# Kernel tuning notes

Measured on AMD Instinct MI355X. Metric: run time of the kernel, lower is better.

Reference implementation:

```python
import jax, jax.numpy as jnp
import numpy as np

K = 5       # kernel_size
UP = 2      # up_factor
EPS = 1e-5  # BatchNorm eps (eval mode)


def _conv(x, w, pad, dil=1):
    return jax.lax.conv_general_dilated(
        x, w, (1, 1), [(pad, pad), (pad, pad)], rhs_dilation=(dil, dil),
        dimension_numbers=('NCHW', 'OIHW', 'NCHW'))


def _bn(x, g, b, m, v):
    inv = g / jnp.sqrt(v + EPS)
    return x * inv[:, None, None] + (b - m * inv)[:, None, None]


def _bilinear(x, oh, ow):
    # torch F.interpolate(mode='bilinear', align_corners=False)
    N, C, H, W = x.shape
    def coords(out_s, in_s):
        s = in_s / out_s
        src = (jnp.arange(out_s, dtype=jnp.float32) + 0.5) * s - 0.5
        src = jnp.clip(src, 0.0, in_s - 1)
        i0 = jnp.floor(src).astype(jnp.int32)
        i1 = jnp.minimum(i0 + 1, in_s - 1)
        return i0, i1, src - i0
    y0, y1, wy = coords(oh, H)
    x0, x1, wx = coords(ow, W)
    g = lambda yi, xi: x[:, :, yi][:, :, :, xi]  # (N,C,oh,ow)
    top = g(y0, x0) * (1 - wx) + g(y0, x1) * wx
    bot = g(y1, x0) * (1 - wx) + g(y1, x1) * wx
    return top * (1 - wy)[:, None] + bot * wy[:, None]


def _unfold(x):
    # F.unfold(k=5, pad=2) reshaped to (N, C, K*K, H, W); channel-major (c, kh, kw)
    p = K // 2
    N, C, H, W = x.shape
    xp = jnp.pad(x, ((0, 0), (0, 0), (p, p), (p, p)))
    patches = [xp[:, :, i:i + H, j:j + W] for i in range(K) for j in range(K)]
    return jnp.stack(patches, axis=2)


def setup_inputs() -> dict:
    key = jax.random.key(0)
    ks = jax.random.split(key, 8)
    N, C, H, W = 2, 256, 48, 48
    Cc = C // 4
    Cout = 256
    d = {}
    d['x'] = jax.random.normal(ks[0], (N, C, H, W), dtype=jnp.float32)
    d['compress_w'] = jax.random.normal(ks[1], (Cc, C, 1, 1), dtype=jnp.float32) * 0.05
    d['g1'] = jnp.ones((Cc,), jnp.float32)
    d['b1'] = jnp.zeros((Cc,), jnp.float32)
    d['m1'] = jax.random.normal(ks[2], (Cc,), dtype=jnp.float32) * 0.1
    d['v1'] = jax.random.uniform(ks[3], (Cc,), minval=0.5, maxval=1.5, dtype=jnp.float32)
    d['ke1_w'] = jax.random.normal(ks[4], (Cc, Cc, 3, 3), dtype=jnp.float32) * 0.05
    d['gk'] = jnp.ones((Cc,), jnp.float32)
    d['bk'] = jnp.zeros((Cc,), jnp.float32)
    d['mk'] = jax.random.normal(ks[5], (Cc,), dtype=jnp.float32) * 0.1
    d['vk'] = jax.random.uniform(ks[6], (Cc,), minval=0.5, maxval=1.5, dtype=jnp.float32)
    d['ke2_w'] = jax.random.normal(ks[7], (UP * UP * K * K, Cc, 3, 3), dtype=jnp.float32) * 0.05
    d['proj_w'] = jax.random.normal(jax.random.fold_in(key, 10), (Cout, C, 1, 1), dtype=jnp.float32) * 0.05
    d['g2'] = jnp.ones((Cout,), jnp.float32)
    d['b2'] = jnp.zeros((Cout,), jnp.float32)
    d['m2'] = jax.random.normal(jax.random.fold_in(key, 11), (Cout,), dtype=jnp.float32) * 0.1
    d['v2'] = jax.random.uniform(jax.random.fold_in(key, 12), (Cout,), minval=0.5, maxval=1.5, dtype=jnp.float32)
    return d


def reference(x, compress_w, g1, b1, m1, v1, ke1_w, gk, bk, mk, vk, ke2_w,
              proj_w, g2, b2, m2, v2):
    N, C, H, W = x.shape
    oh, ow = H * UP, W * UP
    # kernel prediction branch
    comp = jax.nn.relu(_bn(_conv(x, compress_w, 0), g1, b1, m1, v1))
    k1 = jax.nn.relu(_bn(_conv(comp, ke1_w, 2, dil=2), gk, bk, mk, vk))
    kernel = _conv(k1, ke2_w, 1)                               # (N, UP^2*K^2, H, W)
    kernel = jax.nn.softmax(kernel.reshape(N, UP * UP, K * K, H, W), axis=2)
    # content reassembly
    x_up = jnp.repeat(jnp.repeat(x, UP, axis=2), UP, axis=3)
    x_unf = _unfold(x_up)                                      # (N, C, K^2, oh, ow)
    k_up = _bilinear(kernel.reshape(N, UP * UP * K * K, H, W), oh, ow)
    k_up = k_up.reshape(N, UP * UP, K * K, oh, ow)
    out = jnp.einsum('nckhw,nukhw->nuchw', x_unf, k_up)        # (N, UP^2, C, oh, ow)
    # view (N, UP^2*C, oh, ow) then pixel_shuffle(UP)
    out = out.reshape(N, UP * UP * C, oh, ow)
    out = out.reshape(N, C, UP, UP, oh, ow)
    out = out.transpose(0, 1, 4, 2, 5, 3).reshape(N, C, oh * UP, ow * UP)
    out = jax.nn.relu(_bn(_conv(out, proj_w, 0), g2, b2, m2, v2))
    return out
```

## Files before the change

### kernel.cpp

```cpp
#include <hip/hip_runtime.h>

#define EPSB 1e-5f

typedef __attribute__((ext_vector_type(8))) short bf16x8;
typedef __attribute__((ext_vector_type(4))) float f32x4;

__device__ __forceinline__ unsigned short f2b(float f) {
  union { float f; unsigned u; } cv; cv.f = f;
  unsigned r = cv.u + 0x7FFFu + ((cv.u >> 16) & 1u);
  return (unsigned short)(r >> 16);
}

__global__ __launch_bounds__(256) void k_head(
    const float* __restrict__ x, const float* __restrict__ cw,
    const float* __restrict__ g1, const float* __restrict__ b1,
    const float* __restrict__ m1, const float* __restrict__ v1,
    const float* __restrict__ k1w, const float* __restrict__ k2w,
    const float* __restrict__ pw,
    unsigned short* __restrict__ comp_t, unsigned short* __restrict__ pwb,
    unsigned short* __restrict__ wt1, unsigned short* __restrict__ wt2) {
  int bid = blockIdx.x, t = threadIdx.x;
  if (bid < 288) {
    __shared__ unsigned short wl[16640];
    for (int f = t; f < 16384; f += 256) {
      int co = f >> 8, ci = f & 255;
      wl[ci * 65 + co] = f2b(cw[f]);
    }
    __syncthreads();
    int idx = bid * 256 + t;
    int co2 = (idx & 31) * 2;
    int pg = idx >> 5;
    int n = pg / 1152;
    int pix0 = (pg % 1152) * 2;
    const float* xp = x + (size_t)n * 256 * 2304 + pix0;
    float a00 = 0.f, a01 = 0.f, a10 = 0.f, a11 = 0.f;
    for (int ci = 0; ci < 256; ++ci) {
      float2 xv = *(const float2*)(xp + (size_t)ci * 2304);
      unsigned pr = *(const unsigned*)&wl[ci * 65 + co2];
      union { unsigned u; float f; } wa, wb;
      wa.u = pr << 16; wb.u = pr & 0xffff0000u;
      a00 = fmaf(xv.x, wa.f, a00); a01 = fmaf(xv.y, wa.f, a01);
      a10 = fmaf(xv.x, wb.f, a10); a11 = fmaf(xv.y, wb.f, a11);
    }
    float iv0 = g1[co2] / sqrtf(v1[co2] + EPSB);
    float iv1 = g1[co2 + 1] / sqrtf(v1[co2 + 1] + EPSB);
    float c0b = b1[co2] - m1[co2] * iv0;
    float c1b = b1[co2 + 1] - m1[co2 + 1] * iv1;
    float o00 = fmaxf(fmaf(a00, iv0, c0b), 0.f), o01 = fmaxf(fmaf(a01, iv0, c0b), 0.f);
    float o10 = fmaxf(fmaf(a10, iv1, c1b), 0.f), o11 = fmaxf(fmaf(a11, iv1, c1b), 0.f);
    int r = pix0 / 48, c = pix0 % 48;
    unsigned short* ob = comp_t + ((size_t)n * 2704 + (r + 2) * 52 + (c + 2)) * 64 + co2;
    *(unsigned*)&ob[0]  = (unsigned)f2b(o00) | ((unsigned)f2b(o10) << 16);
    *(unsigned*)&ob[64] = (unsigned)f2b(o01) | ((unsigned)f2b(o11) << 16);
  } else if (bid < 388) {
    int i = (bid - 288) * 256 + t;
    int n = i / 12800, r = i % 12800;
    int bp = r >> 5, c32 = r & 31;
    int rr, cc;
    if (bp < 104) { rr = bp / 52; cc = bp % 52; }
    else if (bp >= 296) { rr = 50 + (bp - 296) / 52; cc = (bp - 296) % 52; }
    else { int q = bp - 104; rr = 2 + (q >> 2); int c4 = q & 3; cc = (c4 < 2) ? c4 : c4 + 48; }
    ((unsigned*)comp_t)[((size_t)n * 2704 + rr * 52 + cc) * 32 + c32] = 0u;
  } else {
    int i2 = (bid - 388) * 256 + t;
    if (i2 < 65536) {
      pwb[i2] = f2b(pw[i2]);
    } else if (i2 < 102400) {
      int a = i2 - 65536;
      int co = a / 576, k = a % 576, tap = k >> 6, ci = k & 63;
      wt1[a] = f2b(k1w[co * 576 + ci * 9 + tap]);
    } else {
      int c2 = i2 - 102400;
      int co = c2 / 576, k = c2 % 576, tap = k >> 6, ci = k & 63;
      wt2[c2] = (co < 100) ? f2b(k2w[co * 576 + ci * 9 + tap]) : (unsigned short)0;
    }
  }
}

__global__ __launch_bounds__(128) void k_ke1(
    const unsigned short* __restrict__ comp_t, const unsigned short* __restrict__ wt1,
    const float* __restrict__ gk, const float* __restrict__ bk,
    const float* __restrict__ mk, const float* __restrict__ vk,
    unsigned short* __restrict__ k1_t) {
  int bid = blockIdx.x, t = threadIdx.x;
  if (bid >= 192) {
    int j = (bid - 192) * 128 + t;
    int n = j / 6272, r = j % 6272;
    int bp = r >> 5, c32 = r & 31;
    int rr, cc;
    if (bp < 50) { rr = 0; cc = bp; }
    else if (bp >= 146) { rr = 49; cc = bp - 146; }
    else { int q = bp - 50; rr = 1 + (q >> 1); cc = (q & 1) * 49; }
    ((unsigned*)k1_t)[((size_t)n * 2500 + rr * 50 + cc) * 32 + c32] = 0u;
    return;
  }
  __shared__ unsigned short sA[16640];
  int n = bid / 96, rem = bid % 96;
  int y = rem >> 1, coh = rem & 1;
  const unsigned short* src = comp_t + ((size_t)n * 52 + y) * 52 * 64;
  for (int f = t; f < 2080; f += 128) {
    int g = f >> 3, ci0 = (f & 7) * 8;
    int cc = g % 52, rr = g / 52;
    bf16x8 vv = *(const bf16x8*)&src[(rr * 52 + cc) * 64 + ci0];
    int ba = (((rr * 52 + cc) * 64 + ci0) * 2) ^ ((cc & 7) << 4);
    *(bf16x8*)((char*)sA + ba) = vv;
  }
  __syncthreads();
  int wid = t >> 6, l = t & 63, l15 = l & 15, lg = l >> 4;
  f32x4 acc[3];
  acc[0] = acc[1] = acc[2] = (f32x4){0.f, 0.f, 0.f, 0.f};
  const unsigned short* arow = wt1 + (size_t)(coh * 32 + wid * 16 + l15) * 576;
#pragma unroll
  for (int kbi = 0; kbi < 18; ++kbi) {
    int tap = kbi >> 1;
    int ky = tap / 3, kx = tap % 3;
    int ci0 = (kbi & 1) * 32 + lg * 8;
    bf16x8 afr = *(const bf16x8*)&arow[kbi * 32 + lg * 8];
#pragma unroll
    for (int nt = 0; nt < 3; ++nt) {
      int col = nt * 16 + l15 + 2 * kx;
      int ba = (((2 * ky * 52 + col) * 64 + ci0) * 2) ^ ((col & 7) << 4);
      bf16x8 bfr = *(const bf16x8*)((char*)sA + ba);
      acc[nt] = __builtin_amdgcn_mfma_f32_16x16x32_bf16(afr, bfr, acc[nt], 0, 0, 0);
    }
  }
  unsigned short* dst = k1_t + ((size_t)n * 50 + (y + 1)) * 50 * 64;
  int co0 = coh * 32 + wid * 16 + lg * 4;
  float s0 = gk[co0] / sqrtf(vk[co0] + EPSB);
  float s1 = gk[co0 + 1] / sqrtf(vk[co0 + 1] + EPSB);
  float s2 = gk[co0 + 2] / sqrtf(vk[co0 + 2] + EPSB);
  float s3 = gk[co0 + 3] / sqrtf(vk[co0 + 3] + EPSB);
  float d0 = bk[co0] - mk[co0] * s0;
  float d1 = bk[co0 + 1] - mk[co0 + 1] * s1;
  float d2 = bk[co0 + 2] - mk[co0 + 2] * s2;
  float d3 = bk[co0 + 3] - mk[co0 + 3] * s3;
#pragma unroll
  for (int nt = 0; nt < 3; ++nt) {
    int px = nt * 16 + l15;
    ushort4 pk;
    pk.x = f2b(fmaxf(fmaf(acc[nt][0], s0, d0), 0.f));
    pk.y = f2b(fmaxf(fmaf(acc[nt][1], s1, d1), 0.f));
    pk.z = f2b(fmaxf(fmaf(acc[nt][2], s2, d2), 0.f));
    pk.w = f2b(fmaxf(fmaf(acc[nt][3], s3, d3), 0.f));
    *(ushort4*)&dst[(px + 1) * 64 + co0] = pk;
  }
}

__global__ __launch_bounds__(128) void k_ke2(
    const unsigned short* __restrict__ k1_t, const unsigned short* __restrict__ wt2,
    float* __restrict__ kern_t) {
  __shared__ unsigned short sA[9600];
  int bid = blockIdx.x, t = threadIdx.x;
  int n = bid / 96, rem = bid % 96;
  int y = rem >> 1, coh = rem & 1;
  const unsigned short* src = k1_t + ((size_t)n * 50 + y) * 50 * 64;
  for (int f = t; f < 1200; f += 128) {
    int g = f >> 3, ci0 = (f & 7) * 8;
    int cc = g % 50, rr = g / 50;
    bf16x8 vv = *(const bf16x8*)&src[(rr * 50 + cc) * 64 + ci0];
    int ba = (((rr * 50 + cc) * 64 + ci0) * 2) ^ ((cc & 7) << 4);
    *(bf16x8*)((char*)sA + ba) = vv;
  }
  __syncthreads();
  int wid = t >> 6, l = t & 63, l15 = l & 15, lg = l >> 4;
  f32x4 acc[2][3];
#pragma unroll
  for (int mi = 0; mi < 2; ++mi)
#pragma unroll
    for (int nt = 0; nt < 3; ++nt) acc[mi][nt] = (f32x4){0.f, 0.f, 0.f, 0.f};
#pragma unroll
  for (int kbi = 0; kbi < 18; ++kbi) {
    int tap = kbi >> 1;
    int ky = tap / 3, kx = tap % 3;
    int ci0 = (kbi & 1) * 32 + lg * 8;
    bf16x8 afr[2];
#pragma unroll
    for (int mi = 0; mi < 2; ++mi)
      afr[mi] = *(const bf16x8*)&wt2[(size_t)(coh * 64 + (wid * 2 + mi) * 16 + l15) * 576 + kbi * 32 + lg * 8];
#pragma unroll
    for (int nt = 0; nt < 3; ++nt) {
      int col = nt * 16 + l15 + kx;
      int ba = (((ky * 50 + col) * 64 + ci0) * 2) ^ ((col & 7) << 4);
      bf16x8 bfr = *(const bf16x8*)((char*)sA + ba);
      acc[0][nt] = __builtin_amdgcn_mfma_f32_16x16x32_bf16(afr[0], bfr, acc[0][nt], 0, 0, 0);
      acc[1][nt] = __builtin_amdgcn_mfma_f32_16x16x32_bf16(afr[1], bfr, acc[1][nt], 0, 0, 0);
    }
  }
#pragma unroll
  for (int mi = 0; mi < 2; ++mi) {
    int co0 = coh * 64 + (wid * 2 + mi) * 16 + lg * 4;
    if (co0 < 112) {
#pragma unroll
      for (int nt = 0; nt < 3; ++nt) {
        int px = nt * 16 + l15;
        float4 vv = {acc[mi][nt][0], acc[mi][nt][1], acc[mi][nt][2], acc[mi][nt][3]};
        *(float4*)&kern_t[((size_t)n * 2304 + y * 48 + px) * 112 + co0] = vv;
      }
    }
  }
}

__device__ __forceinline__ void compute_write(
    const float* __restrict__ xls, const float* __restrict__ w9s,
    unsigned short* __restrict__ ftbuf,
    int c, int ch, int u, int jb, int cb, int crr) {
  int p = c & 1;
  const float* xc0 = &xls[((2 * p + 0) * 64 + ch) * 35];
  const float* xc1 = &xls[((2 * p + 1) * 64 + ch) * 35];
  int cbase = jb >> 1;
  float w60[3][6], w61[3][6];
#pragma unroll
  for (int ry = 0; ry < 3; ++ry)
#pragma unroll
    for (int cc = 0; cc < 6; ++cc) {
      w60[ry][cc] = xc0[ry * 11 + cbase + cc];
      w61[ry][cc] = xc1[ry * 11 + cbase + cc];
    }
  const float* wrow = &w9s[((c >> 1) * 16 + jb) * 48 + u * 12];
#pragma unroll
  for (int jj = 0; jj < 8; ++jj) {
    const float* wt = wrow + jj * 48;
    float4 wa = *(const float4*)wt;
    float4 wb = *(const float4*)(wt + 4);
    float w8 = wt[8];
    int cs = jj >> 1;
    float a0 = w60[0][cs] * wa.x;
    a0 = fmaf(w60[0][cs + 1], wa.y, a0);
    a0 = fmaf(w60[0][cs + 2], wa.z, a0);
    a0 = fmaf(w60[1][cs],     wa.w, a0);
    a0 = fmaf(w60[1][cs + 1], wb.x, a0);
    a0 = fmaf(w60[1][cs + 2], wb.y, a0);
    a0 = fmaf(w60[2][cs],     wb.z, a0);
    a0 = fmaf(w60[2][cs + 1], wb.w, a0);
    a0 = fmaf(w60[2][cs + 2], w8,   a0);
    int px0 = 2 * (jb + jj);
    ftbuf[px0 * 256 + ((cb ^ (px0 & 7)) * 8 + crr)] = f2b(a0);
    float a1 = w61[0][cs] * wa.x;
    a1 = fmaf(w61[0][cs + 1], wa.y, a1);
    a1 = fmaf(w61[0][cs + 2], wa.z, a1);
    a1 = fmaf(w61[1][cs],     wa.w, a1);
    a1 = fmaf(w61[1][cs + 1], wb.x, a1);
    a1 = fmaf(w61[1][cs + 2], wb.y, a1);
    a1 = fmaf(w61[2][cs],     wb.z, a1);
    a1 = fmaf(w61[2][cs + 1], wb.w, a1);
    a1 = fmaf(w61[2][cs + 2], w8,   a1);
    int px1 = px0 + 1;
    ftbuf[px1 * 256 + ((cb ^ (px1 & 7)) * 8 + crr)] = f2b(a1);
  }
}

__global__ __launch_bounds__(512, 4) void k_fused(
    const float* __restrict__ x, const float* __restrict__ kern_t,
    const unsigned short* __restrict__ pwb,
    const float* __restrict__ g2, const float* __restrict__ b2,
    const float* __restrict__ m2, const float* __restrict__ v2,
    float* __restrict__ out) {
  __shared__ __align__(16) char smem[76800];
  float* xls  = (float*)smem;
  float* w9s  = (float*)(smem + 35840);
  float* sb2s = (float*)(smem + 41984);
  unsigned short* finT0 = (unsigned short*)(smem + 44032);
  float* ks   = (float*)(smem + 44032);

  int blk = blockIdx.x;
  int n = blk / 288, r = blk % 288;
  int y48 = r / 6, xt = r % 6;
  int X0 = xt * 32, x480 = xt * 8;
  int t = threadIdx.x;

  if (t < 256) {
    float iv = g2[t] / sqrtf(v2[t] + EPSB);
    sb2s[t] = iv; sb2s[256 + t] = b2[t] - m2[t] * iv;
  }
  for (int f = t; f < 840; f += 512) {
    int slot = f / 280, rem = f % 280;
    int cx = rem / 28, c4 = rem % 28;
    int sy = min(max(y48 + slot - 1, 0), 47);
    int sx = min(max(x480 + cx - 1, 0), 47);
    float4 vv = *(const float4*)&kern_t[((size_t)n * 2304 + sy * 48 + sx) * 112 + c4 * 4];
    *(float4*)&ks[(slot * 10 + cx) * 112 + c4 * 4] = vv;
  }
  const float* xb = x + (size_t)n * 256 * 2304;
  for (int f = t; f < 8448; f += 512) {
    int c = f / 33, rc = f - c * 33;
    int ry = rc / 11, cx = rc - ry * 11;
    int sy = min(max(y48 + ry - 1, 0), 47);
    int sx = min(max(x480 + cx - 1, 0), 47);
    int slot = (c & 3) * 64 + (c >> 2);
    xls[slot * 35 + rc] = xb[(size_t)c * 2304 + sy * 48 + sx];
  }
  __syncthreads();

  {
    int s = t & 3, tri = t >> 2;
    int u = tri & 3, w2l = (tri >> 2) & 15, yhh = tri >> 6;
    int y96 = 2 * y48 + yhh;
    int w2 = xt * 16 + w2l;
    float syf = fminf(fmaxf(y96 * 0.5f - 0.25f, 0.f), 47.f);
    int y0 = (int)syf; float wy = syf - (float)y0; int y1 = min(y0 + 1, 47);
    float sxf = fminf(fmaxf(w2 * 0.5f - 0.25f, 0.f), 47.f);
    int x0 = (int)sxf; float wx = sxf - (float)x0; int x1 = min(x0 + 1, 47);
    int slr = ((s & 2) ? y1 : y0) - y48 + 1;
    int cxr = ((s & 1) ? x1 : x0) - x480 + 1;
    float wgt = ((s & 1) ? wx : 1.f - wx) * ((s & 2) ? wy : 1.f - wy);
    const float* p = &ks[(slr * 10 + cxr) * 112 + u * 25];
    float bl[25], mx = -3.4e38f;
#pragma unroll
    for (int k = 0; k < 25; ++k) { bl[k] = p[k]; mx = fmaxf(mx, bl[k]); }
    float sum = 0.f;
#pragma unroll
    for (int k = 0; k < 25; ++k) { bl[k] = __expf(bl[k] - mx); sum += bl[k]; }
    float rs = wgt / sum;
#pragma unroll
    for (int k = 0; k < 25; ++k) {
      bl[k] *= rs;
      bl[k] += __shfl_xor(bl[k], 1);
      bl[k] += __shfl_xor(bl[k], 2);
    }
    if (s == 0) {
#pragma unroll
      for (int kh = 0; kh < 5; ++kh) {
        bool vy = (unsigned)(y96 + kh - 2) < 96u;
#pragma unroll
        for (int kw = 0; kw < 5; ++kw) {
          bool vx = (unsigned)(w2 + kw - 2) < 96u;
          if (!(vy && vx)) bl[kh * 5 + kw] = 0.f;
        }
      }
      int py = yhh, px_ = w2l & 1;
      float cc0[5], cc1[5], cc2[5];
#pragma unroll
      for (int kh = 0; kh < 5; ++kh) {
        cc0[kh] = px_ ? bl[kh * 5 + 0] : bl[kh * 5 + 0] + bl[kh * 5 + 1];
        cc1[kh] = px_ ? bl[kh * 5 + 1] + bl[kh * 5 + 2] : bl[kh * 5 + 2] + bl[kh * 5 + 3];
        cc2[kh] = px_ ? bl[kh * 5 + 3] + bl[kh * 5 + 4] : bl[kh * 5 + 4];
      }
      float* op = &w9s[(yhh * 16 + w2l) * 48 + u * 12];
      op[0] = py ? cc0[0] : cc0[0] + cc0[1];
      op[1] = py ? cc1[0] : cc1[0] + cc1[1];
      op[2] = py ? cc2[0] : cc2[0] + cc2[1];
      op[3] = py ? cc0[1] + cc0[2] : cc0[2] + cc0[3];
      op[4] = py ? cc1[1] + cc1[2] : cc1[2] + cc1[3];
      op[5] = py ? cc2[1] + cc2[2] : cc2[2] + cc2[3];
      op[6] = py ? cc0[3] + cc0[4] : cc0[4];
      op[7] = py ? cc1[3] + cc1[4] : cc1[4];
      op[8] = py ? cc2[3] + cc2[4] : cc2[4];
    }
  }
  __syncthreads();

  int ci = t & 255, half = t >> 8;
  int u = ci >> 6, ch = ci & 63;
  int cb = ci >> 3, crr = ci & 7;
  int jb = half * 8;
  int wid = t >> 6, l = t & 63, l15 = l & 15, lg = l >> 4;
  const unsigned short* a0p = pwb + (size_t)(wid * 32 + l15) * 256;
  const unsigned short* a1p = a0p + 16 * 256;
  size_t outn = (size_t)n * 256 * 36864;
  int Ybase = 4 * y48;

  compute_write(xls, w9s, finT0, 0, ch, u, jb, cb, crr);
  __syncthreads();

#pragma unroll
  for (int c = 0; c < 4; ++c) {
    f32x4 acc[2][2];
#pragma unroll
    for (int mi = 0; mi < 2; ++mi)
#pragma unroll
      for (int nt = 0; nt < 2; ++nt) acc[mi][nt] = (f32x4){0.f, 0.f, 0.f, 0.f};
#pragma unroll
    for (int kbi = 0; kbi < 8; ++kbi) {
      bf16x8 afr0 = *(const bf16x8*)&a0p[kbi * 32 + lg * 8];
      bf16x8 afr1 = *(const bf16x8*)&a1p[kbi * 32 + lg * 8];
      int cbk = kbi * 4 + lg;
#pragma unroll
      for (int nt = 0; nt < 2; ++nt) {
        int row = nt * 16 + l15;
        bf16x8 bfr = *(const bf16x8*)&finT0[(c & 1) * 8192 + row * 256 + ((cbk ^ (row & 7)) * 8)];
        acc[0][nt] = __builtin_amdgcn_mfma_f32_16x16x32_bf16(afr0, bfr, acc[0][nt], 0, 0, 0);
        acc[1][nt] = __builtin_amdgcn_mfma_f32_16x16x32_bf16(afr1, bfr, acc[1][nt], 0, 0, 0);
      }
    }
    if (c < 3) compute_write(xls, w9s, finT0 + ((c + 1) & 1) * 8192, c + 1, ch, u, jb, cb, crr);
    {
      float* orow = out + outn + (size_t)(Ybase + c) * 192 + X0;
#pragma unroll
      for (int mi = 0; mi < 2; ++mi) {
#pragma unroll
        for (int r4 = 0; r4 < 4; ++r4) {
          int o = (wid * 2 + mi) * 16 + lg * 4 + r4;
          float sc = sb2s[o], bi = sb2s[256 + o];
#pragma unroll
          for (int nt = 0; nt < 2; ++nt) {
            float val = fmaxf(fmaf(acc[mi][nt][r4], sc, bi), 0.f);
            orow[(size_t)o * 36864 + nt * 16 + l15] = val;
          }
        }
      }
    }
    if (c < 3) __syncthreads();
  }
}

extern "C" void kernel_launch(void* const* d_in, const int* in_sizes, int n_in,
                              void* d_out, int out_size, void* d_ws, size_t ws_size,
                              hipStream_t stream) {
  const float* x   = (const float*)d_in[0];
  const float* cw  = (const float*)d_in[1];
  const float* g1  = (const float*)d_in[2];
  const float* b1  = (const float*)d_in[3];
  const float* m1  = (const float*)d_in[4];
  const float* v1  = (const float*)d_in[5];
  const float* k1w = (const float*)d_in[6];
  const float* gk  = (const float*)d_in[7];
  const float* bk  = (const float*)d_in[8];
  const float* mk  = (const float*)d_in[9];
  const float* vk  = (const float*)d_in[10];
  const float* k2w = (const float*)d_in[11];
  const float* pw  = (const float*)d_in[12];
  const float* g2  = (const float*)d_in[13];
  const float* b2  = (const float*)d_in[14];
  const float* m2  = (const float*)d_in[15];
  const float* v2  = (const float*)d_in[16];
  float* out = (float*)d_out;
  float* ws  = (float*)d_ws;

  unsigned short* comp_t = (unsigned short*)ws;
  unsigned short* k1_t   = (unsigned short*)(ws + 173056);
  float* kern_t = ws + 333056;
  unsigned short* pwb = (unsigned short*)(ws + 849152);
  unsigned short* wt1 = (unsigned short*)(ws + 881920);
  unsigned short* wt2 = (unsigned short*)(ws + 900352);

  k_head<<<1076, 256, 0, stream>>>(x, cw, g1, b1, m1, v1, k1w, k2w, pw,
                                   comp_t, pwb, wt1, wt2);
  k_ke1<<<290, 128, 0, stream>>>(comp_t, wt1, gk, bk, mk, vk, k1_t);
  k_ke2<<<192, 128, 0, stream>>>(k1_t, wt2, kern_t);
  k_fused<<<576, 512, 0, stream>>>(x, kern_t, pwb, g2, b2, m2, v2, out);
}
```

Measured before the change: 231.3 us.

## Merge prediction-branch kernels into one cooperative kernel and retile fused reassembly

The three prediction-branch kernels (compress conv, dilated 3x3 conv, 3x3 kernel conv) are merged into a single cooperative launch of 256 blocks that uses grid-wide syncs between stages. This removes two kernel launches and their inter-kernel gaps. The ke1 and ke2 stages now give each block a full output row with 256 threads instead of splitting output channels across two blocks, so only 96 of the 256 blocks do MFMA work in those stages. The fused reassembly kernel also packs the 9-tap weights more tightly, processes two output rows per MFMA pass with four N-tiles instead of one row with double buffering, and uses a sliding register window for the 3x3 input taps.

Result: slower. 287.9 us (+24.5%).

```diff
diff --git a/kernel.cpp b/kernel.cpp
--- a/kernel.cpp
+++ b/kernel.cpp
@@ -1,4 +1,7 @@
 #include <hip/hip_runtime.h>
+#include <hip/hip_cooperative_groups.h>
+
+namespace cg = cooperative_groups;
 
 #define EPSB 1e-5f
 
@@ -11,32 +14,37 @@
   return (unsigned short)(r >> 16);
 }
 
-__global__ __launch_bounds__(256) void k_head(
+__global__ __launch_bounds__(256) void k_pred(
     const float* __restrict__ x, const float* __restrict__ cw,
     const float* __restrict__ g1, const float* __restrict__ b1,
     const float* __restrict__ m1, const float* __restrict__ v1,
-    const float* __restrict__ k1w, const float* __restrict__ k2w,
-    const float* __restrict__ pw,
-    unsigned short* __restrict__ comp_t, unsigned short* __restrict__ pwb,
-    unsigned short* __restrict__ wt1, unsigned short* __restrict__ wt2) {
+    const float* __restrict__ k1w,
+    const float* __restrict__ gk, const float* __restrict__ bk,
+    const float* __restrict__ mk, const float* __restrict__ vk,
+    const float* __restrict__ k2w, const float* __restrict__ pw,
+    unsigned short* __restrict__ comp_t, unsigned short* __restrict__ k1_t,
+    float* __restrict__ kern_t,
+    unsigned short* __restrict__ pwb, unsigned short* __restrict__ wt1,
+    unsigned short* __restrict__ wt2) {
+  __shared__ unsigned short sh[16896];
+  cg::grid_group grid = cg::this_grid();
   int bid = blockIdx.x, t = threadIdx.x;
-  if (bid < 288) {
-    __shared__ unsigned short wl[16640];
-    for (int f = t; f < 16384; f += 256) {
-      int co = f >> 8, ci = f & 255;
-      wl[ci * 65 + co] = f2b(cw[f]);
-    }
-    __syncthreads();
-    int idx = bid * 256 + t;
-    int co2 = (idx & 31) * 2;
-    int pg = idx >> 5;
+
+  for (int f = t; f < 16384; f += 256) {
+    int co = f >> 8, ci = f & 255;
+    sh[ci * 66 + co] = f2b(cw[f]);
+  }
+  __syncthreads();
+  for (int it = bid * 256 + t; it < 73728; it += 65536) {
+    int co2 = (it & 31) * 2;
+    int pg = it >> 5;
     int n = pg / 1152;
     int pix0 = (pg % 1152) * 2;
     const float* xp = x + (size_t)n * 256 * 2304 + pix0;
     float a00 = 0.f, a01 = 0.f, a10 = 0.f, a11 = 0.f;
     for (int ci = 0; ci < 256; ++ci) {
       float2 xv = *(const float2*)(xp + (size_t)ci * 2304);
-      unsigned pr = *(const unsigned*)&wl[ci * 65 + co2];
+      unsigned pr = *(const unsigned*)&sh[ci * 66 + co2];
       union { unsigned u; float f; } wa, wb;
       wa.u = pr << 16; wb.u = pr & 0xffff0000u;
       a00 = fmaf(xv.x, wa.f, a00); a01 = fmaf(xv.y, wa.f, a01);
@@ -52,17 +60,8 @@
     unsigned short* ob = comp_t + ((size_t)n * 2704 + (r + 2) * 52 + (c + 2)) * 64 + co2;
     *(unsigned*)&ob[0]  = (unsigned)f2b(o00) | ((unsigned)f2b(o10) << 16);
     *(unsigned*)&ob[64] = (unsigned)f2b(o01) | ((unsigned)f2b(o11) << 16);
-  } else if (bid < 388) {
-    int i = (bid - 288) * 256 + t;
-    int n = i / 12800, r = i % 12800;
-    int bp = r >> 5, c32 = r & 31;
-    int rr, cc;
-    if (bp < 104) { rr = bp / 52; cc = bp % 52; }
-    else if (bp >= 296) { rr = 50 + (bp - 296) / 52; cc = (bp - 296) % 52; }
-    else { int q = bp - 104; rr = 2 + (q >> 2); int c4 = q & 3; cc = (c4 < 2) ? c4 : c4 + 48; }
-    ((unsigned*)comp_t)[((size_t)n * 2704 + rr * 52 + cc) * 32 + c32] = 0u;
-  } else {
-    int i2 = (bid - 388) * 256 + t;
+  }
+  for (int i2 = bid * 256 + t; i2 < 176128; i2 += 65536) {
     if (i2 < 65536) {
       pwb[i2] = f2b(pw[i2]);
     } else if (i2 < 102400) {
@@ -75,177 +74,130 @@
       wt2[c2] = (co < 100) ? f2b(k2w[co * 576 + ci * 9 + tap]) : (unsigned short)0;
     }
   }
-}
-
-__global__ __launch_bounds__(128) void k_ke1(
-    const unsigned short* __restrict__ comp_t, const unsigned short* __restrict__ wt1,
-    const float* __restrict__ gk, const float* __restrict__ bk,
-    const float* __restrict__ mk, const float* __restrict__ vk,
-    unsigned short* __restrict__ k1_t) {
-  int bid = blockIdx.x, t = threadIdx.x;
-  if (bid >= 192) {
-    int j = (bid - 192) * 128 + t;
-    int n = j / 6272, r = j % 6272;
-    int bp = r >> 5, c32 = r & 31;
-    int rr, cc;
-    if (bp < 50) { rr = 0; cc = bp; }
-    else if (bp >= 146) { rr = 49; cc = bp - 146; }
-    else { int q = bp - 50; rr = 1 + (q >> 1); cc = (q & 1) * 49; }
-    ((unsigned*)k1_t)[((size_t)n * 2500 + rr * 50 + cc) * 32 + c32] = 0u;
-    return;
-  }
-  __shared__ unsigned short sA[16640];
-  int n = bid / 96, rem = bid % 96;
-  int y = rem >> 1, coh = rem & 1;
-  const unsigned short* src = comp_t + ((size_t)n * 52 + y) * 52 * 64;
-  for (int f = t; f < 2080; f += 128) {
-    int g = f >> 3, ci0 = (f & 7) * 8;
-    int cc = g % 52, rr = g / 52;
-    bf16x8 vv = *(const bf16x8*)&src[(rr * 52 + cc) * 64 + ci0];
-    int ba = (((rr * 52 + cc) * 64 + ci0) * 2) ^ ((cc & 7) << 4);
-    *(bf16x8*)((char*)sA + ba) = vv;
-  }
-  __syncthreads();
-  int wid = t >> 6, l = t & 63, l15 = l & 15, lg = l >> 4;
-  f32x4 acc[3];
-  acc[0] = acc[1] = acc[2] = (f32x4){0.f, 0.f, 0.f, 0.f};
-  const unsigned short* arow = wt1 + (size_t)(coh * 32 + wid * 16 + l15) * 576;
-#pragma unroll
-  for (int kbi = 0; kbi < 18; ++kbi) {
-    int tap = kbi >> 1;
-    int ky = tap / 3, kx = tap % 3;
-    int ci0 = (kbi & 1) * 32 + lg * 8;
-    bf16x8 afr = *(const bf16x8*)&arow[kbi * 32 + lg * 8];
+  {
+    int i = bid * 256 + t;
+    if (i < 25600) {
+      int n = i / 12800, r = i % 12800;
+      int bp = r >> 5, c32 = r & 31;
+      int rr, cc;
+      if (bp < 104) { rr = bp / 52; cc = bp % 52; }
+      else if (bp >= 296) { rr = 50 + (bp - 296) / 52; cc = (bp - 296) % 52; }
+      else { int q = bp - 104; rr = 2 + (q >> 2); int c4 = q & 3; cc = (c4 < 2) ? c4 : c4 + 48; }
+      ((unsigned*)comp_t)[((size_t)n * 2704 + rr * 52 + cc) * 32 + c32] = 0u;
+    }
+  }
+  grid.sync();
+
+  if (bid < 96) {
+    int n = bid / 48, y = bid % 48;
+    const unsigned short* src = comp_t + ((size_t)n * 52 + y) * 52 * 64;
+    for (int f = t; f < 2080; f += 256) {
+      int g = f >> 3, ci0 = (f & 7) * 8;
+      int cc = g % 52, rr = g / 52;
+      bf16x8 vv = *(const bf16x8*)&src[(rr * 52 + cc) * 64 + ci0];
+      int ba = (((rr * 52 + cc) * 64 + ci0) * 2) ^ ((cc & 7) << 4);
+      *(bf16x8*)((char*)sh + ba) = vv;
+    }
+    __syncthreads();
+    int wid = t >> 6, l = t & 63, l15 = l & 15, lg = l >> 4;
+    f32x4 acc[3];
+    acc[0] = acc[1] = acc[2] = (f32x4){0.f, 0.f, 0.f, 0.f};
+    const unsigned short* arow = wt1 + (size_t)(wid * 16 + l15) * 576;
+#pragma unroll
+    for (int kbi = 0; kbi < 18; ++kbi) {
+      int tap = kbi >> 1;
+      int ky = tap / 3, kx = tap % 3;
+      int ci0 = (kbi & 1) * 32 + lg * 8;
+      bf16x8 afr = *(const bf16x8*)&arow[kbi * 32 + lg * 8];
+#pragma unroll
+      for (int nt = 0; nt < 3; ++nt) {
+        int col = nt * 16 + l15 + 2 * kx;
+        int ba = (((2 * ky * 52 + col) * 64 + ci0) * 2) ^ ((col & 7) << 4);
+        bf16x8 bfr = *(const bf16x8*)((char*)sh + ba);
+        acc[nt] = __builtin_amdgcn_mfma_f32_16x16x32_bf16(afr, bfr, acc[nt], 0, 0, 0);
+      }
+    }
+    unsigned short* dst = k1_t + ((size_t)n * 50 + (y + 1)) * 50 * 64;
+    int co0 = wid * 16 + lg * 4;
+    float s0 = gk[co0] / sqrtf(vk[co0] + EPSB);
+    float s1 = gk[co0 + 1] / sqrtf(vk[co0 + 1] + EPSB);
+    float s2 = gk[co0 + 2] / sqrtf(vk[co0 + 2] + EPSB);
+    float s3 = gk[co0 + 3] / sqrtf(vk[co0 + 3] + EPSB);
+    float d0 = bk[co0] - mk[co0] * s0;
+    float d1 = bk[co0 + 1] - mk[co0 + 1] * s1;
+    float d2 = bk[co0 + 2] - mk[co0 + 2] * s2;
+    float d3 = bk[co0 + 3] - mk[co0 + 3] * s3;
 #pragma unroll
     for (int nt = 0; nt < 3; ++nt) {
-      int col = nt * 16 + l15 + 2 * kx;
-      int ba = (((2 * ky * 52 + col) * 64 + ci0) * 2) ^ ((col & 7) << 4);
-      bf16x8 bfr = *(const bf16x8*)((char*)sA + ba);
-      acc[nt] = __builtin_amdgcn_mfma_f32_16x16x32_bf16(afr, bfr, acc[nt], 0, 0, 0);
-    }
-  }
-  unsigned short* dst = k1_t + ((size_t)n * 50 + (y + 1)) * 50 * 64;
-  int co0 = coh * 32 + wid * 16 + lg * 4;
-  float s0 = gk[co0] / sqrtf(vk[co0] + EPSB);
-  float s1 = gk[co0 + 1] / sqrtf(vk[co0 + 1] + EPSB);
-  float s2 = gk[co0 + 2] / sqrtf(vk[co0 + 2] + EPSB);
-  float s3 = gk[co0 + 3] / sqrtf(vk[co0 + 3] + EPSB);
-  float d0 = bk[co0] - mk[co0] * s0;
-  float d1 = bk[co0 + 1] - mk[co0 + 1] * s1;
-  float d2 = bk[co0 + 2] - mk[co0 + 2] * s2;
-  float d3 = bk[co0 + 3] - mk[co0 + 3] * s3;
-#pragma unroll
-  for (int nt = 0; nt < 3; ++nt) {
-    int px = nt * 16 + l15;
-    ushort4 pk;
-    pk.x = f2b(fmaxf(fmaf(acc[nt][0], s0, d0), 0.f));
-    pk.y = f2b(fmaxf(fmaf(acc[nt][1], s1, d1), 0.f));
-    pk.z = f2b(fmaxf(fmaf(acc[nt][2], s2, d2), 0.f));
-    pk.w = f2b(fmaxf(fmaf(acc[nt][3], s3, d3), 0.f));
-    *(ushort4*)&dst[(px + 1) * 64 + co0] = pk;
-  }
-}
-
-__global__ __launch_bounds__(128) void k_ke2(
-    const unsigned short* __restrict__ k1_t, const unsigned short* __restrict__ wt2,
-    float* __restrict__ kern_t) {
-  __shared__ unsigned short sA[9600];
-  int bid = blockIdx.x, t = threadIdx.x;
-  int n = bid / 96, rem = bid % 96;
-  int y = rem >> 1, coh = rem & 1;
-  const unsigned short* src = k1_t + ((size_t)n * 50 + y) * 50 * 64;
-  for (int f = t; f < 1200; f += 128) {
-    int g = f >> 3, ci0 = (f & 7) * 8;
-    int cc = g % 50, rr = g / 50;
-    bf16x8 vv = *(const bf16x8*)&src[(rr * 50 + cc) * 64 + ci0];
-    int ba = (((rr * 50 + cc) * 64 + ci0) * 2) ^ ((cc & 7) << 4);
-    *(bf16x8*)((char*)sA + ba) = vv;
-  }
-  __syncthreads();
-  int wid = t >> 6, l = t & 63, l15 = l & 15, lg = l >> 4;
-  f32x4 acc[2][3];
-#pragma unroll
-  for (int mi = 0; mi < 2; ++mi)
-#pragma unroll
-    for (int nt = 0; nt < 3; ++nt) acc[mi][nt] = (f32x4){0.f, 0.f, 0.f, 0.f};
-#pragma unroll
-  for (int kbi = 0; kbi < 18; ++kbi) {
-    int tap = kbi >> 1;
-    int ky = tap / 3, kx = tap % 3;
-    int ci0 = (kbi & 1) * 32 + lg * 8;
-    bf16x8 afr[2];
+      int px = nt * 16 + l15;
+      ushort4 pk;
+      pk.x = f2b(fmaxf(fmaf(acc[nt][0], s0, d0), 0.f));
+      pk.y = f2b(fmaxf(fmaf(acc[nt][1], s1, d1), 0.f));
+      pk.z = f2b(fmaxf(fmaf(acc[nt][2], s2, d2), 0.f));
+      pk.w = f2b(fmaxf(fmaf(acc[nt][3], s3, d3), 0.f));
+      *(ushort4*)&dst[(px + 1) * 64 + co0] = pk;
+    }
+  } else {
+    int j = (bid - 96) * 256 + t;
+    if (j < 12544) {
+      int n = j / 6272, r = j % 6272;
+      int bp = r >> 5, c32 = r & 31;
+      int rr, cc;
+      if (bp < 50) { rr = 0; cc = bp; }
+      else if (bp >= 146) { rr = 49; cc = bp - 146; }
+      else { int q = bp - 50; rr = 1 + (q >> 1); cc = (q & 1) * 49; }
+      ((unsigned*)k1_t)[((size_t)n * 2500 + rr * 50 + cc) * 32 + c32] = 0u;
+    }
+  }
+  grid.sync();
+
+  if (bid < 96) {
+    int n = bid / 48, y = bid % 48;
+    const unsigned short* src = k1_t + ((size_t)n * 50 + y) * 50 * 64;
+    for (int f = t; f < 1200; f += 256) {
+      int g = f >> 3, ci0 = (f & 7) * 8;
+      int cc = g % 50, rr = g / 50;
+      bf16x8 vv = *(const bf16x8*)&src[(rr * 50 + cc) * 64 + ci0];
+      int ba = (((rr * 50 + cc) * 64 + ci0) * 2) ^ ((cc & 7) << 4);
+      *(bf16x8*)((char*)sh + ba) = vv;
+    }
+    __syncthreads();
+    int wid = t >> 6, l = t & 63, l15 = l & 15, lg = l >> 4;
+    f32x4 acc[2][3];
 #pragma unroll
     for (int mi = 0; mi < 2; ++mi)
-      afr[mi] = *(const bf16x8*)&wt2[(size_t)(coh * 64 + (wid * 2 + mi) * 16 + l15) * 576 + kbi * 32 + lg * 8];
-#pragma unroll
-    for (int nt = 0; nt < 3; ++nt) {
-      int col = nt * 16 + l15 + kx;
-      int ba = (((ky * 50 + col) * 64 + ci0) * 2) ^ ((col & 7) << 4);
-      bf16x8 bfr = *(const bf16x8*)((char*)sA + ba);
-      acc[0][nt] = __builtin_amdgcn_mfma_f32_16x16x32_bf16(afr[0], bfr, acc[0][nt], 0, 0, 0);
-      acc[1][nt] = __builtin_amdgcn_mfma_f32_16x16x32_bf16(afr[1], bfr, acc[1][nt], 0, 0, 0);
-    }
-  }
-#pragma unroll
-  for (int mi = 0; mi < 2; ++mi) {
-    int co0 = coh * 64 + (wid * 2 + mi) * 16 + lg * 4;
-    if (co0 < 112) {
+#pragma unroll
+      for (int nt = 0; nt < 3; ++nt) acc[mi][nt] = (f32x4){0.f, 0.f, 0.f, 0.f};
+#pragma unroll
+    for (int kbi = 0; kbi < 18; ++kbi) {
+      int tap = kbi >> 1;
+      int ky = tap / 3, kx = tap % 3;
+      int ci0 = (kbi & 1) * 32 + lg * 8;
+      bf16x8 afr[2];
+#pragma unroll
+      for (int mi = 0; mi < 2; ++mi)
+        afr[mi] = *(const bf16x8*)&wt2[(size_t)((wid * 2 + mi) * 16 + l15) * 576 + kbi * 32 + lg * 8];
 #pragma unroll
       for (int nt = 0; nt < 3; ++nt) {
-        int px = nt * 16 + l15;
-        float4 vv = {acc[mi][nt][0], acc[mi][nt][1], acc[mi][nt][2], acc[mi][nt][3]};
-        *(float4*)&kern_t[((size_t)n * 2304 + y * 48 + px) * 112 + co0] = vv;
-      }
-    }
-  }
-}
-
-__device__ __forceinline__ void compute_write(
-    const float* __restrict__ xls, const float* __restrict__ w9s,
-    unsigned short* __restrict__ ftbuf,
-    int c, int ch, int u, int jb, int cb, int crr) {
-  int p = c & 1;
-  const float* xc0 = &xls[((2 * p + 0) * 64 + ch) * 35];
-  const float* xc1 = &xls[((2 * p + 1) * 64 + ch) * 35];
-  int cbase = jb >> 1;
-  float w60[3][6], w61[3][6];
-#pragma unroll
-  for (int ry = 0; ry < 3; ++ry)
-#pragma unroll
-    for (int cc = 0; cc < 6; ++cc) {
-      w60[ry][cc] = xc0[ry * 11 + cbase + cc];
-      w61[ry][cc] = xc1[ry * 11 + cbase + cc];
-    }
-  const float* wrow = &w9s[((c >> 1) * 16 + jb) * 48 + u * 12];
-#pragma unroll
-  for (int jj = 0; jj < 8; ++jj) {
-    const float* wt = wrow + jj * 48;
-    float4 wa = *(const float4*)wt;
-    float4 wb = *(const float4*)(wt + 4);
-    float w8 = wt[8];
-    int cs = jj >> 1;
-    float a0 = w60[0][cs] * wa.x;
-    a0 = fmaf(w60[0][cs + 1], wa.y, a0);
-    a0 = fmaf(w60[0][cs + 2], wa.z, a0);
-    a0 = fmaf(w60[1][cs],     wa.w, a0);
-    a0 = fmaf(w60[1][cs + 1], wb.x, a0);
-    a0 = fmaf(w60[1][cs + 2], wb.y, a0);
-    a0 = fmaf(w60[2][cs],     wb.z, a0);
-    a0 = fmaf(w60[2][cs + 1], wb.w, a0);
-    a0 = fmaf(w60[2][cs + 2], w8,   a0);
-    int px0 = 2 * (jb + jj);
-    ftbuf[px0 * 256 + ((cb ^ (px0 & 7)) * 8 + crr)] = f2b(a0);
-    float a1 = w61[0][cs] * wa.x;
-    a1 = fmaf(w61[0][cs + 1], wa.y, a1);
-    a1 = fmaf(w61[0][cs + 2], wa.z, a1);
-    a1 = fmaf(w61[1][cs],     wa.w, a1);
-    a1 = fmaf(w61[1][cs + 1], wb.x, a1);
-    a1 = fmaf(w61[1][cs + 2], wb.y, a1);
-    a1 = fmaf(w61[2][cs],     wb.z, a1);
-    a1 = fmaf(w61[2][cs + 1], wb.w, a1);
-    a1 = fmaf(w61[2][cs + 2], w8,   a1);
-    int px1 = px0 + 1;
-    ftbuf[px1 * 256 + ((cb ^ (px1 & 7)) * 8 + crr)] = f2b(a1);
+        int col = nt * 16 + l15 + kx;
+        int ba = (((ky * 50 + col) * 64 + ci0) * 2) ^ ((col & 7) << 4);
+        bf16x8 bfr = *(const bf16x8*)((char*)sh + ba);
+        acc[0][nt] = __builtin_amdgcn_mfma_f32_16x16x32_bf16(afr[0], bfr, acc[0][nt], 0, 0, 0);
+        acc[1][nt] = __builtin_amdgcn_mfma_f32_16x16x32_bf16(afr[1], bfr, acc[1][nt], 0, 0, 0);
+      }
+    }
+#pragma unroll
+    for (int mi = 0; mi < 2; ++mi) {
+      int co0 = (wid * 2 + mi) * 16 + lg * 4;
+      if (co0 < 112) {
+#pragma unroll
+        for (int nt = 0; nt < 3; ++nt) {
+          int px = nt * 16 + l15;
+          float4 vv = {acc[mi][nt][0], acc[mi][nt][1], acc[mi][nt][2], acc[mi][nt][3]};
+          *(float4*)&kern_t[((size_t)n * 2304 + y * 48 + px) * 112 + co0] = vv;
+        }
+      }
+    }
   }
 }
 
@@ -258,8 +210,8 @@
   __shared__ __align__(16) char smem[76800];
   float* xls  = (float*)smem;
   float* w9s  = (float*)(smem + 35840);
-  float* sb2s = (float*)(smem + 41984);
-  unsigned short* finT0 = (unsigned short*)(smem + 44032);
+  float* sb2s = (float*)(smem + 40448);
+  unsigned short* finT = (unsigned short*)(smem + 44032);
   float* ks   = (float*)(smem + 44032);
 
   int blk = blockIdx.x;
@@ -335,7 +287,7 @@
         cc1[kh] = px_ ? bl[kh * 5 + 1] + bl[kh * 5 + 2] : bl[kh * 5 + 2] + bl[kh * 5 + 3];
         cc2[kh] = px_ ? bl[kh * 5 + 3] + bl[kh * 5 + 4] : bl[kh * 5 + 4];
       }
-      float* op = &w9s[(yhh * 16 + w2l) * 48 + u * 12];
+      float* op = &w9s[(yhh * 16 + w2l) * 36 + u * 9];
       op[0] = py ? cc0[0] : cc0[0] + cc0[1];
       op[1] = py ? cc1[0] : cc1[0] + cc1[1];
       op[2] = py ? cc2[0] : cc2[0] + cc2[1];
@@ -349,57 +301,87 @@
   }
   __syncthreads();
 
-  int ci = t & 255, half = t >> 8;
+  int ci = t & 255, rY = t >> 8;
   int u = ci >> 6, ch = ci & 63;
   int cb = ci >> 3, crr = ci & 7;
-  int jb = half * 8;
   int wid = t >> 6, l = t & 63, l15 = l & 15, lg = l >> 4;
   const unsigned short* a0p = pwb + (size_t)(wid * 32 + l15) * 256;
   const unsigned short* a1p = a0p + 16 * 256;
   size_t outn = (size_t)n * 256 * 36864;
   int Ybase = 4 * y48;
 
-  compute_write(xls, w9s, finT0, 0, ch, u, jb, cb, crr);
-  __syncthreads();
-
-#pragma unroll
-  for (int c = 0; c < 4; ++c) {
-    f32x4 acc[2][2];
+#pragma unroll
+  for (int c = 0; c < 2; ++c) {
+    {
+      const float* xc0 = &xls[((rY * 2 + 0) * 64 + ch) * 35];
+      const float* xc1 = &xls[((rY * 2 + 1) * 64 + ch) * 35];
+      float xw0[9], xw1[9];
+#pragma unroll
+      for (int ry = 0; ry < 3; ++ry)
+#pragma unroll
+        for (int cx = 0; cx < 3; ++cx) {
+          xw0[ry * 3 + cx] = xc0[ry * 11 + cx];
+          xw1[ry * 3 + cx] = xc1[ry * 11 + cx];
+        }
+#pragma unroll
+      for (int j = 0; j < 16; ++j) {
+        if (j >= 2 && (j & 1) == 0) {
+          int nc = (j >> 1) + 2;
+#pragma unroll
+          for (int ry = 0; ry < 3; ++ry) {
+            xw0[ry*3+0]=xw0[ry*3+1]; xw0[ry*3+1]=xw0[ry*3+2]; xw0[ry*3+2]=xc0[ry*11+nc];
+            xw1[ry*3+0]=xw1[ry*3+1]; xw1[ry*3+1]=xw1[ry*3+2]; xw1[ry*3+2]=xc1[ry*11+nc];
+          }
+        }
+        const float* wt = &w9s[(c * 16 + j) * 36 + u * 9];
+        float a0 = 0.f, a1 = 0.f;
+#pragma unroll
+        for (int k9 = 0; k9 < 9; ++k9) {
+          float wv = wt[k9];
+          a0 = fmaf(xw0[k9], wv, a0);
+          a1 = fmaf(xw1[k9], wv, a1);
+        }
+        int px0 = rY * 32 + 2 * j, px1 = px0 + 1;
+        finT[px0 * 256 + ((cb ^ (px0 & 7)) * 8 + crr)] = f2b(a0);
+        finT[px1 * 256 + ((cb ^ (px1 & 7)) * 8 + crr)] = f2b(a1);
+      }
+    }
+    __syncthreads();
+
+    f32x4 acc[2][4];
 #pragma unroll
     for (int mi = 0; mi < 2; ++mi)
 #pragma unroll
-      for (int nt = 0; nt < 2; ++nt) acc[mi][nt] = (f32x4){0.f, 0.f, 0.f, 0.f};
+      for (int nt = 0; nt < 4; ++nt) acc[mi][nt] = (f32x4){0.f, 0.f, 0.f, 0.f};
 #pragma unroll
     for (int kbi = 0; kbi < 8; ++kbi) {
       bf16x8 afr0 = *(const bf16x8*)&a0p[kbi * 32 + lg * 8];
       bf16x8 afr1 = *(const bf16x8*)&a1p[kbi * 32 + lg * 8];
       int cbk = kbi * 4 + lg;
 #pragma unroll
-      for (int nt = 0; nt < 2; ++nt) {
+      for (int nt = 0; nt < 4; ++nt) {
         int row = nt * 16 + l15;
-        bf16x8 bfr = *(const bf16x8*)&finT0[(c & 1) * 8192 + row * 256 + ((cbk ^ (row & 7)) * 8)];
+        bf16x8 bfr = *(const bf16x8*)&finT[row * 256 + ((cbk ^ (row & 7)) * 8)];
         acc[0][nt] = __builtin_amdgcn_mfma_f32_16x16x32_bf16(afr0, bfr, acc[0][nt], 0, 0, 0);
         acc[1][nt] = __builtin_amdgcn_mfma_f32_16x16x32_bf16(afr1, bfr, acc[1][nt], 0, 0, 0);
       }
     }
-    if (c < 3) compute_write(xls, w9s, finT0 + ((c + 1) & 1) * 8192, c + 1, ch, u, jb, cb, crr);
-    {
-      float* orow = out + outn + (size_t)(Ybase + c) * 192 + X0;
-#pragma unroll
-      for (int mi = 0; mi < 2; ++mi) {
-#pragma unroll
-        for (int r4 = 0; r4 < 4; ++r4) {
-          int o = (wid * 2 + mi) * 16 + lg * 4 + r4;
-          float sc = sb2s[o], bi = sb2s[256 + o];
-#pragma unroll
-          for (int nt = 0; nt < 2; ++nt) {
-            float val = fmaxf(fmaf(acc[mi][nt][r4], sc, bi), 0.f);
-            orow[(size_t)o * 36864 + nt * 16 + l15] = val;
-          }
-        }
-      }
-    }
-    if (c < 3) __syncthreads();
+#pragma unroll
+    for (int mi = 0; mi < 2; ++mi) {
+#pragma unroll
+      for (int r4 = 0; r4 < 4; ++r4) {
+        int o = (wid * 2 + mi) * 16 + lg * 4 + r4;
+        float sc = sb2s[o], bi = sb2s[256 + o];
+#pragma unroll
+        for (int nt = 0; nt < 4; ++nt) {
+          int px = nt * 16 + l15;
+          int Yl = c * 2 + (px >> 5), Xl = px & 31;
+          float val = fmaxf(fmaf(acc[mi][nt][r4], sc, bi), 0.f);
+          out[outn + (size_t)o * 36864 + (size_t)(Ybase + Yl) * 192 + X0 + Xl] = val;
+        }
+      }
+    }
+    if (c == 0) __syncthreads();
   }
 }
 
@@ -433,9 +415,14 @@
   unsigned short* wt1 = (unsigned short*)(ws + 881920);
   unsigned short* wt2 = (unsigned short*)(ws + 900352);
 
-  k_head<<<1076, 256, 0, stream>>>(x, cw, g1, b1, m1, v1, k1w, k2w, pw,
-                                   comp_t, pwb, wt1, wt2);
-  k_ke1<<<290, 128, 0, stream>>>(comp_t, wt1, gk, bk, mk, vk, k1_t);
-  k_ke2<<<192, 128, 0, stream>>>(k1_t, wt2, kern_t);
+  void* args[] = {
+    (void*)&x, (void*)&cw, (void*)&g1, (void*)&b1, (void*)&m1, (void*)&v1,
+    (void*)&k1w, (void*)&gk, (void*)&bk, (void*)&mk, (void*)&vk,
+    (void*)&k2w, (void*)&pw,
+    (void*)&comp_t, (void*)&k1_t, (void*)&kern_t,
+    (void*)&pwb, (void*)&wt1, (void*)&wt2
+  };
+  hipLaunchCooperativeKernel((const void*)k_pred, dim3(256), dim3(256), args, 0, stream);
+
   k_fused<<<576, 512, 0, stream>>>(x, kern_t, pwb, g2, b2, m2, v2, out);
 }
```
